# Kernel tuning notes

Measured on AMD Instinct MI355X. Metric: run time of the kernel, lower is better.

Reference implementation:

```python
import jax, jax.numpy as jnp
import numpy as np

EPS = 1e-5
CONV_THRESHOLD = 0.0


def setup_inputs() -> dict:
    key = jax.random.key(0)
    ks = jax.random.split(key, 16)
    B, F = 65536, 256
    H1, H2 = 1024, 512
    d_in = F + 1  # raw features + 1 scalar conv feature
    inp = {
        "x": jax.random.normal(ks[0], (B, F), dtype=jnp.float32),
        # layer 1: Linear(d_in, H1) + BatchNorm1d(H1)
        "W1": jax.random.normal(ks[1], (d_in, H1), dtype=jnp.float32) * (1.0 / np.sqrt(d_in)),
        "b1": jax.random.normal(ks[2], (H1,), dtype=jnp.float32) * 0.01,
        "g1": jnp.ones((H1,), jnp.float32) + 0.1 * jax.random.normal(ks[3], (H1,), dtype=jnp.float32),
        "be1": jax.random.normal(ks[4], (H1,), dtype=jnp.float32) * 0.01,
        "m1": jax.random.normal(ks[5], (H1,), dtype=jnp.float32) * 0.1,
        "v1": jax.random.uniform(ks[6], (H1,), dtype=jnp.float32, minval=0.5, maxval=1.5),
        # layer 2: Linear(H1, H2) + BatchNorm1d(H2)
        "W2": jax.random.normal(ks[7], (H1, H2), dtype=jnp.float32) * (1.0 / np.sqrt(H1)),
        "b2": jax.random.normal(ks[8], (H2,), dtype=jnp.float32) * 0.01,
        "g2": jnp.ones((H2,), jnp.float32) + 0.1 * jax.random.normal(ks[9], (H2,), dtype=jnp.float32),
        "be2": jax.random.normal(ks[10], (H2,), dtype=jnp.float32) * 0.01,
        "m2": jax.random.normal(ks[11], (H2,), dtype=jnp.float32) * 0.1,
        "v2": jax.random.uniform(ks[12], (H2,), dtype=jnp.float32, minval=0.5, maxval=1.5),
        # output head: Linear(H2, 1)
        "W3": jax.random.normal(ks[13], (H2, 1), dtype=jnp.float32) * (1.0 / np.sqrt(H2)),
        "b3": jax.random.normal(ks[14], (1,), dtype=jnp.float32) * 0.01,
    }
    return inp


def _bn(h, g, be, m, v):
    # eval-mode BatchNorm1d with running statistics
    return g * (h - m) * jax.lax.rsqrt(v + EPS) + be


def reference(x, W1, b1, g1, be1, m1, v1, W2, b2, g2, be2, m2, v2, W3, b3):
    # Batched replacement of the per-sample numpy threshold conv:
    # the Conv filter reduces the whole sample patch with a mean and thresholds it,
    # producing one binary scalar feature per sample.  [B, 1]
    conv_feat = jnp.where(jnp.mean(x, axis=1, keepdims=True) > CONV_THRESHOLD, 1.0, 0.0).astype(x.dtype)
    h = jnp.concatenate([x, conv_feat], axis=1)  # [B, F+1]
    h = jax.nn.relu(_bn(h @ W1 + b1, g1, be1, m1, v1))  # [B, H1]
    h = jax.nn.relu(_bn(h @ W2 + b2, g2, be2, m2, v2))  # [B, H2]
    return jax.nn.sigmoid(h @ W3 + b3)  # [B, 1]
```

## Files before the change

kernel.cpp:

```cpp
#include <hip/hip_runtime.h>
#include <hip/hip_bf16.h>
#include <cstdint>
#include <cstddef>

typedef __bf16 bf16_t;
typedef bf16_t bf16x8 __attribute__((ext_vector_type(8)));
typedef bf16_t bf16x4 __attribute__((ext_vector_type(4)));
typedef float f32x4 __attribute__((ext_vector_type(4)));

#define BN_EPS 1e-5f

__device__ __forceinline__ void async_load16(const bf16_t* g, bf16_t* lds) {
  __builtin_amdgcn_global_load_lds(
      (__attribute__((address_space(1))) uint32_t*)(g),
      (__attribute__((address_space(3))) uint32_t*)(lds),
      16, 0, 0);
}

__global__ void prep_kernel(const float* __restrict__ x, bf16_t* __restrict__ xb,
                            float* __restrict__ convf, float* __restrict__ outacc,
                            const float* __restrict__ W1, const float* __restrict__ W2,
                            const float* b1, const float* g1, const float* be1,
                            const float* m1, const float* v1,
                            const float* b2, const float* g2, const float* be2,
                            const float* m2, const float* v2,
                            bf16_t* __restrict__ W1T, bf16_t* __restrict__ W2T,
                            float* s1, float* t1, float* s2, float* t2,
                            float* w1last) {
  const int blk = blockIdx.x;
  if (blk < 16384) {
    int lane = threadIdx.x & 63;
    int w = threadIdx.x >> 6;
    int row = blk * 4 + w;
    const float4 v = *(const float4*)(x + (size_t)row * 256 + lane * 4);
    float s = v.x + v.y + v.z + v.w;
    bf16x4 o = {(bf16_t)v.x, (bf16_t)v.y, (bf16_t)v.z, (bf16_t)v.w};
    *(bf16x4*)(xb + (size_t)row * 256 + lane * 4) = o;
#pragma unroll
    for (int off = 32; off >= 1; off >>= 1) s += __shfl_down(s, off);
    if (lane == 0) convf[row] = (s > 0.0f) ? 1.0f : 0.0f;
    if (threadIdx.x < 4) outacc[blk * 4 + threadIdx.x] = 0.0f;
  } else if (blk < 16576) {
    const int b = blk - 16384;
    const float* src;
    bf16_t* dst;
    int R, C, bx, by;
    if (b < 64) { src = W1; dst = W1T; R = 256; C = 1024; bx = b & 15; by = b >> 4; }
    else        { src = W2; dst = W2T; R = 1024; C = 512; bx = (b - 64) & 7; by = (b - 64) >> 3; }
    __shared__ bf16_t tile[64][66];
    const int r0 = by * 64, c0 = bx * 64;
    const int tc = threadIdx.x & 63;
    const int tr4 = threadIdx.x >> 6;
#pragma unroll
    for (int i = 0; i < 16; ++i) {
      int r = i * 4 + tr4;
      tile[r][tc] = (bf16_t)src[(size_t)(r0 + r) * C + c0 + tc];
    }
    __syncthreads();
#pragma unroll
    for (int i = 0; i < 16; ++i) {
      int rr = i * 4 + tr4;
      dst[(size_t)(c0 + rr) * R + r0 + tc] = tile[tc][rr];
    }
  } else {
    int i = (blk - 16576) * 256 + threadIdx.x;
    if (i < 1024) {
      float s = g1[i] * rsqrtf(v1[i] + BN_EPS);
      s1[i] = s;
      t1[i] = be1[i] - m1[i] * s + b1[i] * s;
      w1last[i] = W1[256 * 1024 + i];
    }
    if (i < 512) {
      float s = g2[i] * rsqrtf(v2[i] + BN_EPS);
      s2[i] = s;
      t2[i] = be2[i] - m2[i] * s + b2[i] * s;
    }
  }
}

__global__ __launch_bounds__(256, 2) void gemm1_kernel(
    const bf16_t* __restrict__ xb, const bf16_t* __restrict__ W1T,
    const float* __restrict__ s1, const float* __restrict__ t1,
    const float* __restrict__ convf, const float* __restrict__ w1last,
    bf16_t* __restrict__ h1) {
  __shared__ __align__(16) bf16_t As[128 * 256];
  __shared__ __align__(16) bf16_t Bs[2][128 * 32];

  const int tid = threadIdx.x;
  const int lane = tid & 63;
  const int w = tid >> 6;
  const int p = w >> 1;
  const int h = w & 1;
  const int l15 = lane & 15;
  const int quad = lane >> 4;
  const int mTile = blockIdx.x * 128;

  {
    const int rsub = lane >> 5;
    const int c = lane & 31;
#pragma unroll
    for (int i = 0; i < 16; ++i) {
      int row = w * 32 + i * 2 + rsub;
      bf16x8 v = *(const bf16x8*)(xb + (size_t)(mTile + row) * 256 + c * 8);
      *(bf16x8*)&As[row * 256 + (c ^ (row & 7)) * 8] = v;
    }
  }

  const float b3dummy = 0.f; (void)b3dummy;

  for (int j = 0; j < 4; ++j) {
    const int colbase = (p * 4 + j) * 128;
    f32x4 acc[4][8];
#pragma unroll
    for (int i = 0; i < 4; ++i)
#pragma unroll
      for (int t = 0; t < 8; ++t) {
        f32x4 z = {0.f, 0.f, 0.f, 0.f};
        acc[i][t] = z;
      }

    const bf16_t* gB = W1T + (size_t)(colbase + h * 64 + (lane >> 2)) * 256 + (lane & 3) * 8;
    bf16_t* lB = Bs[p] + (h * 64) * 32;

    for (int ks = 0; ks < 8; ++ks) {
      __syncthreads();
#pragma unroll
      for (int i = 0; i < 4; ++i)
        async_load16(gB + (size_t)(i * 16) * 256 + ks * 32, lB + (i * 16) * 32);
      __syncthreads();

      bf16x8 af[4], bfr[8];
#pragma unroll
      for (int ti = 0; ti < 4; ++ti) {
        int row = h * 64 + ti * 16 + l15;
        af[ti] = *(const bf16x8*)&As[row * 256 + ((ks * 4 + quad) ^ (l15 & 7)) * 8];
      }
#pragma unroll
      for (int tj = 0; tj < 8; ++tj)
        bfr[tj] = *(const bf16x8*)(Bs[p] + (tj * 16 + l15) * 32 + quad * 8);
#pragma unroll
      for (int ti = 0; ti < 4; ++ti)
#pragma unroll
        for (int tj = 0; tj < 8; ++tj)
          acc[ti][tj] = __builtin_amdgcn_mfma_f32_16x16x32_bf16(af[ti], bfr[tj], acc[ti][tj], 0, 0, 0);
    }

    float sc[8], tc[8], wl[8];
#pragma unroll
    for (int tj = 0; tj < 8; ++tj) {
      int c = colbase + tj * 16 + l15;
      sc[tj] = s1[c];
      tc[tj] = t1[c];
      wl[tj] = w1last[c];
    }
#pragma unroll
    for (int ti = 0; ti < 4; ++ti)
#pragma unroll
      for (int r = 0; r < 4; ++r) {
        int row = mTile + h * 64 + ti * 16 + quad * 4 + r;
        float cf = convf[row];
        size_t base = (size_t)row * 1024 + colbase;
#pragma unroll
        for (int tj = 0; tj < 8; ++tj) {
          float z = acc[ti][tj][r] + cf * wl[tj];
          z = fmaxf(z * sc[tj] + tc[tj], 0.f);
          h1[base + tj * 16 + l15] = (bf16_t)z;
        }
      }
  }
}

__global__ __launch_bounds__(256, 2) void gemm2_head_kernel(
    const bf16_t* __restrict__ A, const bf16_t* __restrict__ BT,
    const float* __restrict__ sN, const float* __restrict__ tN,
    const float* __restrict__ W3, float* __restrict__ outacc) {
  constexpr int K = 1024;
  __shared__ __align__(16) bf16_t As[256 * 32];
  __shared__ __align__(16) bf16_t Bs[128 * 32];

  const int b = blockIdx.x;
  const int mTile = ((b >> 5) * 8 + (b & 7)) * 256;
  const int nTile = ((b >> 3) & 3) * 128;

  const int tid = threadIdx.x;
  const int lane = tid & 63;
  const int w = tid >> 6;
  const int l15 = lane & 15;
  const int quad = lane >> 4;
  const int sRow = lane >> 2;
  const int sCol = (lane & 3) * 8;

  const bf16_t* gA = A + (size_t)(mTile + w * 64 + sRow) * K + sCol;
  const bf16_t* gB = BT + (size_t)(nTile + w * 32 + sRow) * K + sCol;
  bf16_t* lA = As + (w * 64) * 32;
  bf16_t* lB = Bs + (w * 32) * 32;

  f32x4 acc[4][8];
#pragma unroll
  for (int i = 0; i < 4; ++i)
#pragma unroll
    for (int j = 0; j < 8; ++j) {
      f32x4 z = {0.f, 0.f, 0.f, 0.f};
      acc[i][j] = z;
    }

  for (int k0 = 0; k0 < K; k0 += 32) {
    async_load16(gA + k0, lA);
    async_load16(gA + (size_t)16 * K + k0, lA + 16 * 32);
    async_load16(gA + (size_t)32 * K + k0, lA + 32 * 32);
    async_load16(gA + (size_t)48 * K + k0, lA + 48 * 32);
    async_load16(gB + k0, lB);
    async_load16(gB + (size_t)16 * K + k0, lB + 16 * 32);
    __syncthreads();

    bf16x8 af[4], bfr[8];
#pragma unroll
    for (int t = 0; t < 4; ++t)
      af[t] = *(const bf16x8*)(As + (w * 64 + t * 16 + l15) * 32 + quad * 8);
#pragma unroll
    for (int t = 0; t < 8; ++t)
      bfr[t] = *(const bf16x8*)(Bs + (t * 16 + l15) * 32 + quad * 8);
#pragma unroll
    for (int ti = 0; ti < 4; ++ti)
#pragma unroll
      for (int tj = 0; tj < 8; ++tj)
        acc[ti][tj] = __builtin_amdgcn_mfma_f32_16x16x32_bf16(af[ti], bfr[tj], acc[ti][tj], 0, 0, 0);
    __syncthreads();
  }

  float sc[8], tc[8], w3c[8];
#pragma unroll
  for (int tj = 0; tj < 8; ++tj) {
    int c = nTile + tj * 16 + l15;
    sc[tj] = sN[c];
    tc[tj] = tN[c];
    w3c[tj] = W3[c];
  }
#pragma unroll
  for (int ti = 0; ti < 4; ++ti)
#pragma unroll
    for (int r = 0; r < 4; ++r) {
      float p = 0.f;
#pragma unroll
      for (int tj = 0; tj < 8; ++tj) {
        float z = fmaxf(acc[ti][tj][r] * sc[tj] + tc[tj], 0.f);
        p += z * w3c[tj];
      }
#pragma unroll
      for (int m = 1; m <= 8; m <<= 1) p += __shfl_xor(p, m);
      if (l15 == 0)
        atomicAdd(outacc + mTile + w * 64 + ti * 16 + quad * 4 + r, p);
    }
}

__global__ void sigmoid_kernel(float* __restrict__ out, const float* __restrict__ b3) {
  int i = blockIdx.x * 256 + threadIdx.x;
  float z = out[i] + b3[0];
  out[i] = 1.0f / (1.0f + expf(-z));
}

extern "C" void kernel_launch(void* const* d_in, const int* in_sizes, int n_in,
                              void* d_out, int out_size, void* d_ws, size_t ws_size,
                              hipStream_t stream) {
  const float* x = (const float*)d_in[0];
  const float* W1 = (const float*)d_in[1];
  const float* b1 = (const float*)d_in[2];
  const float* g1 = (const float*)d_in[3];
  const float* be1 = (const float*)d_in[4];
  const float* m1 = (const float*)d_in[5];
  const float* v1 = (const float*)d_in[6];
  const float* W2 = (const float*)d_in[7];
  const float* b2 = (const float*)d_in[8];
  const float* g2 = (const float*)d_in[9];
  const float* be2 = (const float*)d_in[10];
  const float* m2 = (const float*)d_in[11];
  const float* v2 = (const float*)d_in[12];
  const float* W3 = (const float*)d_in[13];
  const float* b3 = (const float*)d_in[14];
  float* out = (float*)d_out;

  char* p = (char*)d_ws;
  bf16_t* h1 = (bf16_t*)p;    p += (size_t)65536 * 1024 * 2;
  bf16_t* xb = (bf16_t*)p;    p += (size_t)65536 * 256 * 2;
  bf16_t* W1T = (bf16_t*)p;   p += (size_t)1024 * 256 * 2;
  bf16_t* W2T = (bf16_t*)p;   p += (size_t)512 * 1024 * 2;
  float* convf = (float*)p;   p += (size_t)65536 * 4;
  float* w1last = (float*)p;  p += 1024 * 4;
  float* s1 = (float*)p;      p += 1024 * 4;
  float* t1 = (float*)p;      p += 1024 * 4;
  float* s2 = (float*)p;      p += 512 * 4;
  float* t2 = (float*)p;      p += 512 * 4;

  prep_kernel<<<16580, 256, 0, stream>>>(x, xb, convf, out,
                                         W1, W2, b1, g1, be1, m1, v1,
                                         b2, g2, be2, m2, v2,
                                         W1T, W2T, s1, t1, s2, t2, w1last);

  gemm1_kernel<<<512, 256, 0, stream>>>(xb, W1T, s1, t1, convf, w1last, h1);
  gemm2_head_kernel<<<1024, 256, 0, stream>>>(h1, W2T, s2, t2, W3, out);

  sigmoid_kernel<<<256, 256, 0, stream>>>(out, b3);
}
```

Baseline: 259.1 us.

## Fuse x conversion into GEMM1 and run MLP as one cooperative kernel

```diff
diff --git a/kernel.cpp b/kernel.cpp
--- a/kernel.cpp
+++ b/kernel.cpp
@@ -1,11 +1,13 @@
 #include <hip/hip_runtime.h>
 #include <hip/hip_bf16.h>
+#include <hip/hip_cooperative_groups.h>
 #include <cstdint>
 #include <cstddef>
 
+namespace cg = cooperative_groups;
+
 typedef __bf16 bf16_t;
 typedef bf16_t bf16x8 __attribute__((ext_vector_type(8)));
-typedef bf16_t bf16x4 __attribute__((ext_vector_type(4)));
 typedef float f32x4 __attribute__((ext_vector_type(4)));
 
 #define BN_EPS 1e-5f
@@ -17,31 +19,16 @@
       16, 0, 0);
 }
 
-__global__ void prep_kernel(const float* __restrict__ x, bf16_t* __restrict__ xb,
-                            float* __restrict__ convf, float* __restrict__ outacc,
-                            const float* __restrict__ W1, const float* __restrict__ W2,
-                            const float* b1, const float* g1, const float* be1,
-                            const float* m1, const float* v1,
-                            const float* b2, const float* g2, const float* be2,
-                            const float* m2, const float* v2,
-                            bf16_t* __restrict__ W1T, bf16_t* __restrict__ W2T,
-                            float* s1, float* t1, float* s2, float* t2,
-                            float* w1last) {
-  const int blk = blockIdx.x;
-  if (blk < 16384) {
-    int lane = threadIdx.x & 63;
-    int w = threadIdx.x >> 6;
-    int row = blk * 4 + w;
-    const float4 v = *(const float4*)(x + (size_t)row * 256 + lane * 4);
-    float s = v.x + v.y + v.z + v.w;
-    bf16x4 o = {(bf16_t)v.x, (bf16_t)v.y, (bf16_t)v.z, (bf16_t)v.w};
-    *(bf16x4*)(xb + (size_t)row * 256 + lane * 4) = o;
-#pragma unroll
-    for (int off = 32; off >= 1; off >>= 1) s += __shfl_down(s, off);
-    if (lane == 0) convf[row] = (s > 0.0f) ? 1.0f : 0.0f;
-    if (threadIdx.x < 4) outacc[blk * 4 + threadIdx.x] = 0.0f;
-  } else if (blk < 16576) {
-    const int b = blk - 16384;
+__global__ void prep_weights_kernel(const float* __restrict__ W1, const float* __restrict__ W2,
+                                    const float* b1, const float* g1, const float* be1,
+                                    const float* m1, const float* v1,
+                                    const float* b2, const float* g2, const float* be2,
+                                    const float* m2, const float* v2,
+                                    bf16_t* __restrict__ W1T, bf16_t* __restrict__ W2T,
+                                    float* s1, float* t1, float* s2, float* t2,
+                                    float* w1last) {
+  const int b = blockIdx.x;
+  if (b < 192) {
     const float* src;
     bf16_t* dst;
     int R, C, bx, by;
@@ -63,37 +50,32 @@
       dst[(size_t)(c0 + rr) * R + r0 + tc] = tile[tc][rr];
     }
   } else {
-    int i = (blk - 16576) * 256 + threadIdx.x;
-    if (i < 1024) {
+    for (int i = threadIdx.x; i < 1024; i += 256) {
       float s = g1[i] * rsqrtf(v1[i] + BN_EPS);
       s1[i] = s;
       t1[i] = be1[i] - m1[i] * s + b1[i] * s;
       w1last[i] = W1[256 * 1024 + i];
-    }
-    if (i < 512) {
-      float s = g2[i] * rsqrtf(v2[i] + BN_EPS);
-      s2[i] = s;
-      t2[i] = be2[i] - m2[i] * s + b2[i] * s;
-    }
-  }
-}
-
-__global__ __launch_bounds__(256, 2) void gemm1_kernel(
-    const bf16_t* __restrict__ xb, const bf16_t* __restrict__ W1T,
+      if (i < 512) {
+        float s2v = g2[i] * rsqrtf(v2[i] + BN_EPS);
+        s2[i] = s2v;
+        t2[i] = be2[i] - m2[i] * s2v + b2[i] * s2v;
+      }
+    }
+  }
+}
+
+__device__ __forceinline__ void gemm1_body(
+    const float* __restrict__ x, const bf16_t* __restrict__ W1T,
     const float* __restrict__ s1, const float* __restrict__ t1,
-    const float* __restrict__ convf, const float* __restrict__ w1last,
-    bf16_t* __restrict__ h1) {
-  __shared__ __align__(16) bf16_t As[128 * 256];
-  __shared__ __align__(16) bf16_t Bs[2][128 * 32];
-
-  const int tid = threadIdx.x;
-  const int lane = tid & 63;
-  const int w = tid >> 6;
+    const float* __restrict__ w1last, bf16_t* __restrict__ h1,
+    unsigned char* smem, int mTile, int lane, int w) {
+  bf16_t* As = (bf16_t*)smem;
+  bf16_t* BsBase = (bf16_t*)(smem + 65536);
+  float* convs = (float*)(smem + 65536);
+  const int l15 = lane & 15;
+  const int quad = lane >> 4;
   const int p = w >> 1;
   const int h = w & 1;
-  const int l15 = lane & 15;
-  const int quad = lane >> 4;
-  const int mTile = blockIdx.x * 128;
 
   {
     const int rsub = lane >> 5;
@@ -101,12 +83,25 @@
 #pragma unroll
     for (int i = 0; i < 16; ++i) {
       int row = w * 32 + i * 2 + rsub;
-      bf16x8 v = *(const bf16x8*)(xb + (size_t)(mTile + row) * 256 + c * 8);
-      *(bf16x8*)&As[row * 256 + (c ^ (row & 7)) * 8] = v;
-    }
-  }
-
-  const float b3dummy = 0.f; (void)b3dummy;
+      const float* gx = x + (size_t)(mTile + row) * 256 + c * 8;
+      const float4 a = *(const float4*)gx;
+      const float4 bq = *(const float4*)(gx + 4);
+      float s = a.x + a.y + a.z + a.w + bq.x + bq.y + bq.z + bq.w;
+      bf16x8 v = {(bf16_t)a.x, (bf16_t)a.y, (bf16_t)a.z, (bf16_t)a.w,
+                  (bf16_t)bq.x, (bf16_t)bq.y, (bf16_t)bq.z, (bf16_t)bq.w};
+      *(bf16x8*)(As + row * 256 + (c ^ (row & 7)) * 8) = v;
+#pragma unroll
+      for (int m = 1; m <= 16; m <<= 1) s += __shfl_xor(s, m);
+      if (c == 0) convs[row] = (s > 0.0f) ? 1.0f : 0.0f;
+    }
+  }
+  __syncthreads();
+  float cf[4][4];
+#pragma unroll
+  for (int ti = 0; ti < 4; ++ti)
+#pragma unroll
+    for (int r = 0; r < 4; ++r)
+      cf[ti][r] = convs[h * 64 + ti * 16 + quad * 4 + r];
 
   for (int j = 0; j < 4; ++j) {
     const int colbase = (p * 4 + j) * 128;
@@ -120,7 +115,7 @@
       }
 
     const bf16_t* gB = W1T + (size_t)(colbase + h * 64 + (lane >> 2)) * 256 + (lane & 3) * 8;
-    bf16_t* lB = Bs[p] + (h * 64) * 32;
+    bf16_t* lB = BsBase + p * (128 * 32) + (h * 64) * 32;
 
     for (int ks = 0; ks < 8; ++ks) {
       __syncthreads();
@@ -133,11 +128,11 @@
 #pragma unroll
       for (int ti = 0; ti < 4; ++ti) {
         int row = h * 64 + ti * 16 + l15;
-        af[ti] = *(const bf16x8*)&As[row * 256 + ((ks * 4 + quad) ^ (l15 & 7)) * 8];
+        af[ti] = *(const bf16x8*)(As + row * 256 + ((ks * 4 + quad) ^ (l15 & 7)) * 8);
       }
 #pragma unroll
       for (int tj = 0; tj < 8; ++tj)
-        bfr[tj] = *(const bf16x8*)(Bs[p] + (tj * 16 + l15) * 32 + quad * 8);
+        bfr[tj] = *(const bf16x8*)(BsBase + p * (128 * 32) + (tj * 16 + l15) * 32 + quad * 8);
 #pragma unroll
       for (int ti = 0; ti < 4; ++ti)
 #pragma unroll
@@ -158,11 +153,10 @@
 #pragma unroll
       for (int r = 0; r < 4; ++r) {
         int row = mTile + h * 64 + ti * 16 + quad * 4 + r;
-        float cf = convf[row];
         size_t base = (size_t)row * 1024 + colbase;
 #pragma unroll
         for (int tj = 0; tj < 8; ++tj) {
-          float z = acc[ti][tj][r] + cf * wl[tj];
+          float z = acc[ti][tj][r] + cf[ti][r] * wl[tj];
           z = fmaxf(z * sc[tj] + tc[tj], 0.f);
           h1[base + tj * 16 + l15] = (bf16_t)z;
         }
@@ -170,30 +164,27 @@
   }
 }
 
-__global__ __launch_bounds__(256, 2) void gemm2_head_kernel(
-    const bf16_t* __restrict__ A, const bf16_t* __restrict__ BT,
-    const float* __restrict__ sN, const float* __restrict__ tN,
-    const float* __restrict__ W3, float* __restrict__ outacc) {
-  constexpr int K = 1024;
-  __shared__ __align__(16) bf16_t As[256 * 32];
-  __shared__ __align__(16) bf16_t Bs[128 * 32];
-
-  const int b = blockIdx.x;
-  const int mTile = ((b >> 5) * 8 + (b & 7)) * 256;
-  const int nTile = ((b >> 3) & 3) * 128;
-
-  const int tid = threadIdx.x;
-  const int lane = tid & 63;
-  const int w = tid >> 6;
+__device__ __forceinline__ void gemm2_task_body(
+    const bf16_t* __restrict__ h1, const bf16_t* __restrict__ W2T,
+    const float* __restrict__ s2, const float* __restrict__ t2,
+    const float* __restrict__ W3, float* __restrict__ partials,
+    unsigned char* smem, int task, int lane, int w) {
+  bf16_t* As2 = (bf16_t*)smem;
+  bf16_t* Bs2 = (bf16_t*)(smem + 16384);
   const int l15 = lane & 15;
   const int quad = lane >> 4;
   const int sRow = lane >> 2;
   const int sCol = (lane & 3) * 8;
 
-  const bf16_t* gA = A + (size_t)(mTile + w * 64 + sRow) * K + sCol;
-  const bf16_t* gB = BT + (size_t)(nTile + w * 32 + sRow) * K + sCol;
-  bf16_t* lA = As + (w * 64) * 32;
-  bf16_t* lB = Bs + (w * 32) * 32;
+  const int mt = (task >> 5) * 8 + (task & 7);
+  const int mTile2 = mt * 256;
+  const int nt = (task >> 3) & 3;
+  const int nTile = nt * 128;
+
+  const bf16_t* gA = h1 + (size_t)(mTile2 + w * 64 + sRow) * 1024 + sCol;
+  const bf16_t* gB = W2T + (size_t)(nTile + w * 32 + sRow) * 1024 + sCol;
+  bf16_t* lA = As2 + (w * 64) * 32;
+  bf16_t* lB = Bs2 + (w * 32) * 32;
 
   f32x4 acc[4][8];
 #pragma unroll
@@ -204,22 +195,22 @@
       acc[i][j] = z;
     }
 
-  for (int k0 = 0; k0 < K; k0 += 32) {
+  for (int k0 = 0; k0 < 1024; k0 += 32) {
     async_load16(gA + k0, lA);
-    async_load16(gA + (size_t)16 * K + k0, lA + 16 * 32);
-    async_load16(gA + (size_t)32 * K + k0, lA + 32 * 32);
-    async_load16(gA + (size_t)48 * K + k0, lA + 48 * 32);
+    async_load16(gA + (size_t)16 * 1024 + k0, lA + 16 * 32);
+    async_load16(gA + (size_t)32 * 1024 + k0, lA + 32 * 32);
+    async_load16(gA + (size_t)48 * 1024 + k0, lA + 48 * 32);
     async_load16(gB + k0, lB);
-    async_load16(gB + (size_t)16 * K + k0, lB + 16 * 32);
+    async_load16(gB + (size_t)16 * 1024 + k0, lB + 16 * 32);
     __syncthreads();
 
     bf16x8 af[4], bfr[8];
 #pragma unroll
     for (int t = 0; t < 4; ++t)
-      af[t] = *(const bf16x8*)(As + (w * 64 + t * 16 + l15) * 32 + quad * 8);
+      af[t] = *(const bf16x8*)(As2 + (w * 64 + t * 16 + l15) * 32 + quad * 8);
 #pragma unroll
     for (int t = 0; t < 8; ++t)
-      bfr[t] = *(const bf16x8*)(Bs + (t * 16 + l15) * 32 + quad * 8);
+      bfr[t] = *(const bf16x8*)(Bs2 + (t * 16 + l15) * 32 + quad * 8);
 #pragma unroll
     for (int ti = 0; ti < 4; ++ti)
 #pragma unroll
@@ -232,31 +223,84 @@
 #pragma unroll
   for (int tj = 0; tj < 8; ++tj) {
     int c = nTile + tj * 16 + l15;
-    sc[tj] = sN[c];
-    tc[tj] = tN[c];
+    sc[tj] = s2[c];
+    tc[tj] = t2[c];
     w3c[tj] = W3[c];
   }
 #pragma unroll
   for (int ti = 0; ti < 4; ++ti)
 #pragma unroll
     for (int r = 0; r < 4; ++r) {
-      float p = 0.f;
+      float pv = 0.f;
 #pragma unroll
       for (int tj = 0; tj < 8; ++tj) {
         float z = fmaxf(acc[ti][tj][r] * sc[tj] + tc[tj], 0.f);
-        p += z * w3c[tj];
-      }
-#pragma unroll
-      for (int m = 1; m <= 8; m <<= 1) p += __shfl_xor(p, m);
+        pv += z * w3c[tj];
+      }
+#pragma unroll
+      for (int m = 1; m <= 8; m <<= 1) pv += __shfl_xor(pv, m);
       if (l15 == 0)
-        atomicAdd(outacc + mTile + w * 64 + ti * 16 + quad * 4 + r, p);
-    }
-}
-
-__global__ void sigmoid_kernel(float* __restrict__ out, const float* __restrict__ b3) {
+        partials[(size_t)nt * 65536 + mTile2 + w * 64 + ti * 16 + quad * 4 + r] = pv;
+    }
+}
+
+__global__ __launch_bounds__(256, 2) void gemm1_kernel(
+    const float* __restrict__ x, const bf16_t* __restrict__ W1T,
+    const float* __restrict__ s1, const float* __restrict__ t1,
+    const float* __restrict__ w1last, bf16_t* __restrict__ h1) {
+  __shared__ __align__(16) unsigned char smem[81920];
+  gemm1_body(x, W1T, s1, t1, w1last, h1, smem, blockIdx.x * 128,
+             threadIdx.x & 63, threadIdx.x >> 6);
+}
+
+__global__ __launch_bounds__(256, 2) void gemm2_kernel(
+    const bf16_t* __restrict__ h1, const bf16_t* __restrict__ W2T,
+    const float* __restrict__ s2, const float* __restrict__ t2,
+    const float* __restrict__ W3, float* __restrict__ partials) {
+  __shared__ __align__(16) unsigned char smem[24576];
+  gemm2_task_body(h1, W2T, s2, t2, W3, partials, smem, blockIdx.x,
+                  threadIdx.x & 63, threadIdx.x >> 6);
+}
+
+__global__ void sigmoid_partials_kernel(const float* __restrict__ partials,
+                                        const float* __restrict__ b3,
+                                        float* __restrict__ out) {
   int i = blockIdx.x * 256 + threadIdx.x;
-  float z = out[i] + b3[0];
+  float z = partials[i] + partials[65536 + i] + partials[2 * 65536 + i] +
+            partials[3 * 65536 + i] + b3[0];
   out[i] = 1.0f / (1.0f + expf(-z));
+}
+
+__global__ __launch_bounds__(256, 2) void fused_mlp_coop(
+    const float* __restrict__ x,
+    const bf16_t* __restrict__ W1T, const bf16_t* __restrict__ W2T,
+    const float* __restrict__ s1, const float* __restrict__ t1,
+    const float* __restrict__ w1last,
+    const float* __restrict__ s2, const float* __restrict__ t2,
+    const float* __restrict__ W3, const float* __restrict__ b3,
+    bf16_t* __restrict__ h1, float* __restrict__ partials,
+    float* __restrict__ out) {
+  __shared__ __align__(16) unsigned char smem[81920];
+  cg::grid_group grid = cg::this_grid();
+  const int tid = threadIdx.x;
+  const int lane = tid & 63;
+  const int w = tid >> 6;
+
+  gemm1_body(x, W1T, s1, t1, w1last, h1, smem, blockIdx.x * 128, lane, w);
+
+  grid.sync();
+
+  gemm2_task_body(h1, W2T, s2, t2, W3, partials, smem, blockIdx.x, lane, w);
+  gemm2_task_body(h1, W2T, s2, t2, W3, partials, smem, blockIdx.x + 512, lane, w);
+
+  grid.sync();
+
+  if (tid < 128) {
+    int r = blockIdx.x * 128 + tid;
+    float z = partials[r] + partials[65536 + r] + partials[2 * 65536 + r] +
+              partials[3 * 65536 + r] + b3[0];
+    out[r] = 1.0f / (1.0f + expf(-z));
+  }
 }
 
 extern "C" void kernel_launch(void* const* d_in, const int* in_sizes, int n_in,
@@ -280,24 +324,41 @@
   float* out = (float*)d_out;
 
   char* p = (char*)d_ws;
-  bf16_t* h1 = (bf16_t*)p;    p += (size_t)65536 * 1024 * 2;
-  bf16_t* xb = (bf16_t*)p;    p += (size_t)65536 * 256 * 2;
-  bf16_t* W1T = (bf16_t*)p;   p += (size_t)1024 * 256 * 2;
-  bf16_t* W2T = (bf16_t*)p;   p += (size_t)512 * 1024 * 2;
-  float* convf = (float*)p;   p += (size_t)65536 * 4;
-  float* w1last = (float*)p;  p += 1024 * 4;
-  float* s1 = (float*)p;      p += 1024 * 4;
-  float* t1 = (float*)p;      p += 1024 * 4;
-  float* s2 = (float*)p;      p += 512 * 4;
-  float* t2 = (float*)p;      p += 512 * 4;
-
-  prep_kernel<<<16580, 256, 0, stream>>>(x, xb, convf, out,
-                                         W1, W2, b1, g1, be1, m1, v1,
-                                         b2, g2, be2, m2, v2,
-                                         W1T, W2T, s1, t1, s2, t2, w1last);
-
-  gemm1_kernel<<<512, 256, 0, stream>>>(xb, W1T, s1, t1, convf, w1last, h1);
-  gemm2_head_kernel<<<1024, 256, 0, stream>>>(h1, W2T, s2, t2, W3, out);
-
-  sigmoid_kernel<<<256, 256, 0, stream>>>(out, b3);
-}
+  bf16_t* h1 = (bf16_t*)p;       p += (size_t)65536 * 1024 * 2;
+  float* partials = (float*)p;   p += (size_t)4 * 65536 * 4;
+  bf16_t* W1T = (bf16_t*)p;      p += (size_t)1024 * 256 * 2;
+  bf16_t* W2T = (bf16_t*)p;      p += (size_t)512 * 1024 * 2;
+  float* w1last = (float*)p;     p += 1024 * 4;
+  float* s1 = (float*)p;         p += 1024 * 4;
+  float* t1 = (float*)p;         p += 1024 * 4;
+  float* s2 = (float*)p;         p += 512 * 4;
+  float* t2 = (float*)p;         p += 512 * 4;
+
+  prep_weights_kernel<<<193, 256, 0, stream>>>(W1, W2, b1, g1, be1, m1, v1,
+                                               b2, g2, be2, m2, v2,
+                                               W1T, W2T, s1, t1, s2, t2, w1last);
+
+  int dev = 0;
+  (void)hipGetDevice(&dev);
+  int coopOk = 0;
+  (void)hipDeviceGetAttribute(&coopOk, hipDeviceAttributeCooperativeLaunch, dev);
+  int numCU = 0;
+  (void)hipDeviceGetAttribute(&numCU, hipDeviceAttributeMultiprocessorCount, dev);
+  int maxBlk = 0;
+  (void)hipOccupancyMaxActiveBlocksPerMultiprocessor(&maxBlk, fused_mlp_coop, 256, 0);
+
+  bool useCoop = (coopOk != 0) && ((long)maxBlk * (long)numCU >= 512L);
+  if (useCoop) {
+    void* args[] = {(void*)&x, (void*)&W1T, (void*)&W2T, (void*)&s1, (void*)&t1,
+                    (void*)&w1last, (void*)&s2, (void*)&t2, (void*)&W3, (void*)&b3,
+                    (void*)&h1, (void*)&partials, (void*)&out};
+    hipError_t e = hipLaunchCooperativeKernel((const void*)fused_mlp_coop,
+                                              dim3(512), dim3(256), args, 0, stream);
+    if (e != hipSuccess) useCoop = false;
+  }
+  if (!useCoop) {
+    gemm1_kernel<<<512, 256, 0, stream>>>(x, W1T, s1, t1, w1last, h1);
+    gemm2_kernel<<<1024, 256, 0, stream>>>(h1, W2T, s2, t2, W3, partials);
+    sigmoid_partials_kernel<<<256, 256, 0, stream>>>(partials, b3, out);
+  }
+}
```

After: 247.9 us. 1.05x faster.
